# Optimization experiments

Hardware: AMD Instinct MI355X
Metric: run time of the kernel (lower is better)

## Reference

```python
import jax, jax.numpy as jnp
import numpy as np

RANK = 8
ALPHA = 16.0
SCALING = ALPHA / RANK  # LoRA scaling alpha/rank
B, T, P, C = 8, 16, 197, 1024


def setup_inputs() -> dict:
    key = jax.random.key(0)
    k = jax.random.split(key, 8)
    hidden_states = jax.random.normal(k[0], (B, T, P, C), jnp.float32)
    frame_mask = jnp.ones((B, T), jnp.float32)
    # kaiming_uniform_(a=sqrt(5)) on an (out,in) Linear -> U(-1/sqrt(in), 1/sqrt(in))
    s_down = 1.0 / np.sqrt(C).astype(np.float32)
    down_w = jax.random.uniform(k[1], (RANK, C), jnp.float32, -s_down, s_down)
    # PyTorch LSTM default init: U(-1/sqrt(hidden), 1/sqrt(hidden)) for all params
    s_l = 1.0 / np.sqrt(RANK).astype(np.float32)
    w_ih = jax.random.uniform(k[2], (4 * RANK, RANK), jnp.float32, -s_l, s_l)
    w_hh = jax.random.uniform(k[3], (4 * RANK, RANK), jnp.float32, -s_l, s_l)
    b_ih = jax.random.uniform(k[4], (4 * RANK,), jnp.float32, -s_l, s_l)
    b_hh = jax.random.uniform(k[5], (4 * RANK,), jnp.float32, -s_l, s_l)
    # original zero-inits up; use small random so the reference output is non-trivial
    up_w = jax.random.normal(k[6], (C, RANK), jnp.float32) * 0.02
    return {
        "hidden_states": hidden_states,
        "num_frames": T,
        "frame_mask": frame_mask,
        "down_w": down_w,
        "w_ih": w_ih,
        "w_hh": w_hh,
        "b_ih": b_ih,
        "b_hh": b_hh,
        "up_w": up_w,
    }


def _lstm(x, w_ih, w_hh, b_ih, b_hh):
    """Single-layer unidirectional LSTM, PyTorch gate order (i,f,g,o).
    x: (T, N, R) time-major. Returns all hidden states (T, N, R)."""
    n, r = x.shape[1], w_hh.shape[1]
    bias = b_ih + b_hh

    def step(carry, x_t):
        h, c = carry
        gates = x_t @ w_ih.T + h @ w_hh.T + bias  # (N, 4R)
        i, f, g, o = jnp.split(gates, 4, axis=-1)
        c = jax.nn.sigmoid(f) * c + jax.nn.sigmoid(i) * jnp.tanh(g)
        h = jax.nn.sigmoid(o) * jnp.tanh(c)
        return (h, c), h

    init = (jnp.zeros((n, r), x.dtype), jnp.zeros((n, r), x.dtype))
    _, hs = jax.lax.scan(step, init, x)
    return hs


def reference(hidden_states, num_frames, frame_mask, down_w, w_ih, w_hh, b_ih, b_hh, up_w):
    b, t, p, c = hidden_states.shape
    assert t == num_frames
    # LoRA down: (B,T,P,C) x (R,C) -> (B,T,P,R)  (dropout is identity in eval)
    red = jnp.einsum('btpc,rc->btpr', hidden_states, down_w)
    red = red * frame_mask[:, :, None, None]
    # temporal LSTM over T, batch = B*P, in rank space
    seq = red.transpose(1, 0, 2, 3).reshape(t, b * p, -1)  # (T, B*P, R)
    hs = _lstm(seq, w_ih, w_hh, b_ih, b_hh)                # (T, B*P, R)
    out = hs.reshape(t, b, p, -1).transpose(1, 0, 2, 3)    # (B, T, P, R)
    out = out * frame_mask[:, :, None, None]
    # LoRA up + scaling: (B,T,P,R) x (C,R) -> (B,T,P,C)
    delta = jnp.einsum('btpr,or->btpo', out, up_w) * SCALING
    return delta
```

## Files before the change

kernel.cpp:

```cpp
#include <hip/hip_runtime.h>
#include <math.h>

#define BB 8
#define TT 16
#define PP 197
#define CC 1024
#define RR 8
#define NROWS (BB * TT * PP)
#define NSEQ  (BB * PP)
#define LORA_SCALE 2.0f

__device__ __forceinline__ float sigf(float x) {
    x = fminf(fmaxf(x, -30.f), 30.f);
    return 1.0f / (1.0f + __expf(-x));
}
__device__ __forceinline__ float tanh_fast(float x) {
    x = fminf(fmaxf(x, -15.f), 15.f);
    float e = __expf(-2.0f * x);
    return (1.0f - e) / (1.0f + e);
}
__device__ __forceinline__ float dot4(const float4& a, const float4& b) {
    return a.x * b.x + a.y * b.y + a.z * b.z + a.w * b.w;
}

__global__ __launch_bounds__(256) void k_down(const float* __restrict__ hs,
                                              const float* __restrict__ dw,
                                              const float* __restrict__ fm,
                                              float* __restrict__ red) {
    const int lane = threadIdx.x & 63;
    const int wave = (blockIdx.x * blockDim.x + threadIdx.x) >> 6;

    float4 w[RR][4];
#pragma unroll
    for (int r = 0; r < RR; ++r)
#pragma unroll
        for (int k = 0; k < 4; ++k)
            w[r][k] = *(const float4*)(dw + r * CC + k * 256 + lane * 4);

    const int row0 = wave * 2;

    float4 xa[4], xb[4];
    const float* rpa = hs + (size_t)row0 * CC;
    const float* rpb = hs + (size_t)(row0 + 1) * CC;
#pragma unroll
    for (int k = 0; k < 4; ++k) xa[k] = *(const float4*)(rpa + k * 256 + lane * 4);
#pragma unroll
    for (int k = 0; k < 4; ++k) xb[k] = *(const float4*)(rpb + k * 256 + lane * 4);

    float acca[RR], accb[RR];
#pragma unroll
    for (int r = 0; r < RR; ++r) {
        float a = 0.f, b = 0.f;
#pragma unroll
        for (int k = 0; k < 4; ++k) {
            a += dot4(xa[k], w[r][k]);
            b += dot4(xb[k], w[r][k]);
        }
        acca[r] = a; accb[r] = b;
    }
#pragma unroll
    for (int d = 32; d >= 1; d >>= 1) {
#pragma unroll
        for (int r = 0; r < RR; ++r) {
            acca[r] += __shfl_xor(acca[r], d, 64);
            accb[r] += __shfl_xor(accb[r], d, 64);
        }
    }
    if (lane == 0) {
        const float ma = fm[row0 / PP];
        const float mb = fm[(row0 + 1) / PP];
        float4* opa = (float4*)(red + (size_t)row0 * RR);
        float4* opb = (float4*)(red + (size_t)(row0 + 1) * RR);
        opa[0] = make_float4(acca[0] * ma, acca[1] * ma, acca[2] * ma, acca[3] * ma);
        opa[1] = make_float4(acca[4] * ma, acca[5] * ma, acca[6] * ma, acca[7] * ma);
        opb[0] = make_float4(accb[0] * mb, accb[1] * mb, accb[2] * mb, accb[3] * mb);
        opb[1] = make_float4(accb[4] * mb, accb[5] * mb, accb[6] * mb, accb[7] * mb);
    }
}

__global__ __launch_bounds__(256) void k_lstm(const float* __restrict__ red,
                                              const float* __restrict__ fm,
                                              const float* __restrict__ w_ih,
                                              const float* __restrict__ w_hh,
                                              const float* __restrict__ b_ih,
                                              const float* __restrict__ b_hh,
                                              float* __restrict__ hsm) {
    const int tid = blockIdx.x * blockDim.x + threadIdx.x;
    const int n = tid >> 3;
    const int r = tid & 7;
    const int lane = threadIdx.x & 63;
    const int grp = lane & 56;
    const bool valid = (n < NSEQ);

    float wi_i[8], wi_f[8], wi_g[8], wi_o[8];
    float wh_i[8], wh_f[8], wh_g[8], wh_o[8];
#pragma unroll
    for (int j = 0; j < 8; ++j) {
        wi_i[j] = w_ih[(r) * 8 + j];
        wi_f[j] = w_ih[(8 + r) * 8 + j];
        wi_g[j] = w_ih[(16 + r) * 8 + j];
        wi_o[j] = w_ih[(24 + r) * 8 + j];
        wh_i[j] = w_hh[(r) * 8 + j];
        wh_f[j] = w_hh[(8 + r) * 8 + j];
        wh_g[j] = w_hh[(16 + r) * 8 + j];
        wh_o[j] = w_hh[(24 + r) * 8 + j];
    }
    const float bi = b_ih[r] + b_hh[r];
    const float bf = b_ih[8 + r] + b_hh[8 + r];
    const float bg = b_ih[16 + r] + b_hh[16 + r];
    const float bo = b_ih[24 + r] + b_hh[24 + r];

    int b = 0, p = 0;
    if (valid) { b = n / PP; p = n - b * PP; }
    const size_t base = ((size_t)b * TT * PP + p) * RR + r;
    const size_t tstride = (size_t)PP * RR;

    float h = 0.f, c = 0.f;
    for (int t = 0; t < TT; ++t) {
        const float x = valid ? red[base + (size_t)t * tstride] : 0.f;
        float gi = bi, gf = bf, gg = bg, go = bo;
#pragma unroll
        for (int j = 0; j < 8; ++j) {
            const float xv = __shfl(x, grp + j, 64);
            const float hv = __shfl(h, grp + j, 64);
            gi += wi_i[j] * xv + wh_i[j] * hv;
            gf += wi_f[j] * xv + wh_f[j] * hv;
            gg += wi_g[j] * xv + wh_g[j] * hv;
            go += wi_o[j] * xv + wh_o[j] * hv;
        }
        c = sigf(gf) * c + sigf(gi) * tanh_fast(gg);
        h = sigf(go) * tanh_fast(c);
        if (valid) hsm[base + (size_t)t * tstride] = h * fm[b * TT + t];
    }
}

__global__ __launch_bounds__(256) void k_up(const float* __restrict__ hsm,
                                            const float* __restrict__ up,
                                            float* __restrict__ out) {
    const int lane = threadIdx.x & 63;
    const int wave = (blockIdx.x * blockDim.x + threadIdx.x) >> 6;

    float4 u[4][4][2];
#pragma unroll
    for (int k = 0; k < 4; ++k)
#pragma unroll
        for (int j = 0; j < 4; ++j) {
            const float* pp = up + (size_t)(k * 256 + lane * 4 + j) * RR;
            u[k][j][0] = *(const float4*)(pp);
            u[k][j][1] = *(const float4*)(pp + 4);
        }

    const int row0 = wave * 2;
#pragma unroll
    for (int rr = 0; rr < 2; ++rr) {
        const int row = row0 + rr;
        const float* hp = hsm + (size_t)row * RR;
        float4 h0 = *(const float4*)(hp);
        float4 h1 = *(const float4*)(hp + 4);
        h0.x *= LORA_SCALE; h0.y *= LORA_SCALE; h0.z *= LORA_SCALE; h0.w *= LORA_SCALE;
        h1.x *= LORA_SCALE; h1.y *= LORA_SCALE; h1.z *= LORA_SCALE; h1.w *= LORA_SCALE;
        float* op = out + (size_t)row * CC;
#pragma unroll
        for (int k = 0; k < 4; ++k) {
            float4 o;
            o.x = dot4(h0, u[k][0][0]) + dot4(h1, u[k][0][1]);
            o.y = dot4(h0, u[k][1][0]) + dot4(h1, u[k][1][1]);
            o.z = dot4(h0, u[k][2][0]) + dot4(h1, u[k][2][1]);
            o.w = dot4(h0, u[k][3][0]) + dot4(h1, u[k][3][1]);
            *(float4*)(op + k * 256 + lane * 4) = o;
        }
    }
}

extern "C" void kernel_launch(void* const* d_in, const int* in_sizes, int n_in,
                              void* d_out, int out_size, void* d_ws, size_t ws_size,
                              hipStream_t stream) {
    const float* hs  = (const float*)d_in[0];
    const float* fm  = (const float*)d_in[2];
    const float* dw  = (const float*)d_in[3];
    const float* wih = (const float*)d_in[4];
    const float* whh = (const float*)d_in[5];
    const float* bih = (const float*)d_in[6];
    const float* bhh = (const float*)d_in[7];
    const float* up  = (const float*)d_in[8];
    float* out = (float*)d_out;

    float* red = (float*)d_ws;
    float* hsm = red + (size_t)NROWS * RR;

    k_down<<<NROWS / 8, 256, 0, stream>>>(hs, dw, fm, red);
    k_lstm<<<(NSEQ * 8 + 255) / 256, 256, 0, stream>>>(red, fm, wih, whh, bih, bhh, hsm);
    k_up<<<NROWS / 8, 256, 0, stream>>>(hsm, up, out);
}
```

Measured before the change: 257.7 us.

## Use persistent grid-stride loops for down/up kernels and prefetch LSTM inputs

The down and up projection kernels become persistent grid-stride loops over 512 blocks, so weights loaded into registers are reused across many rows instead of reloaded per wave. The up kernel also switches to scalar coalesced stores with a 64-stride column layout. The LSTM kernel uses 64-thread blocks so more CUs run it, and prefetches all 16 timesteps of input and mask into registers before the recurrence. The trade-offs are fewer waves in flight to hide memory latency and narrower stores in the up kernel.

```diff
diff --git a/kernel.cpp b/kernel.cpp
--- a/kernel.cpp
+++ b/kernel.cpp
@@ -7,6 +7,7 @@
 #define CC 1024
 #define RR 8
 #define NROWS (BB * TT * PP)
+#define NPAIRS (NROWS / 2)
 #define NSEQ  (BB * PP)
 #define LORA_SCALE 2.0f
 
@@ -28,7 +29,8 @@
                                               const float* __restrict__ fm,
                                               float* __restrict__ red) {
     const int lane = threadIdx.x & 63;
-    const int wave = (blockIdx.x * blockDim.x + threadIdx.x) >> 6;
+    const int wid  = (blockIdx.x * blockDim.x + threadIdx.x) >> 6;
+    const int nw   = (gridDim.x * blockDim.x) >> 6;
 
     float4 w[RR][4];
 #pragma unroll
@@ -37,60 +39,60 @@
         for (int k = 0; k < 4; ++k)
             w[r][k] = *(const float4*)(dw + r * CC + k * 256 + lane * 4);
 
-    const int row0 = wave * 2;
+    for (int pr = wid; pr < NPAIRS; pr += nw) {
+        const int row0 = pr * 2;
+        float4 xa[4], xb[4];
+        const float* rpa = hs + (size_t)row0 * CC;
+        const float* rpb = rpa + CC;
+#pragma unroll
+        for (int k = 0; k < 4; ++k) xa[k] = *(const float4*)(rpa + k * 256 + lane * 4);
+#pragma unroll
+        for (int k = 0; k < 4; ++k) xb[k] = *(const float4*)(rpb + k * 256 + lane * 4);
 
-    float4 xa[4], xb[4];
-    const float* rpa = hs + (size_t)row0 * CC;
-    const float* rpb = hs + (size_t)(row0 + 1) * CC;
-#pragma unroll
-    for (int k = 0; k < 4; ++k) xa[k] = *(const float4*)(rpa + k * 256 + lane * 4);
-#pragma unroll
-    for (int k = 0; k < 4; ++k) xb[k] = *(const float4*)(rpb + k * 256 + lane * 4);
-
-    float acca[RR], accb[RR];
-#pragma unroll
-    for (int r = 0; r < RR; ++r) {
-        float a = 0.f, b = 0.f;
-#pragma unroll
-        for (int k = 0; k < 4; ++k) {
-            a += dot4(xa[k], w[r][k]);
-            b += dot4(xb[k], w[r][k]);
-        }
-        acca[r] = a; accb[r] = b;
-    }
-#pragma unroll
-    for (int d = 32; d >= 1; d >>= 1) {
+        float acca[RR], accb[RR];
 #pragma unroll
         for (int r = 0; r < RR; ++r) {
-            acca[r] += __shfl_xor(acca[r], d, 64);
-            accb[r] += __shfl_xor(accb[r], d, 64);
+            float a = 0.f, b = 0.f;
+#pragma unroll
+            for (int k = 0; k < 4; ++k) {
+                a += dot4(xa[k], w[r][k]);
+                b += dot4(xb[k], w[r][k]);
+            }
+            acca[r] = a; accb[r] = b;
         }
-    }
-    if (lane == 0) {
-        const float ma = fm[row0 / PP];
-        const float mb = fm[(row0 + 1) / PP];
-        float4* opa = (float4*)(red + (size_t)row0 * RR);
-        float4* opb = (float4*)(red + (size_t)(row0 + 1) * RR);
-        opa[0] = make_float4(acca[0] * ma, acca[1] * ma, acca[2] * ma, acca[3] * ma);
-        opa[1] = make_float4(acca[4] * ma, acca[5] * ma, acca[6] * ma, acca[7] * ma);
-        opb[0] = make_float4(accb[0] * mb, accb[1] * mb, accb[2] * mb, accb[3] * mb);
-        opb[1] = make_float4(accb[4] * mb, accb[5] * mb, accb[6] * mb, accb[7] * mb);
+#pragma unroll
+        for (int d = 32; d >= 1; d >>= 1) {
+#pragma unroll
+            for (int r = 0; r < RR; ++r) {
+                acca[r] += __shfl_xor(acca[r], d, 64);
+                accb[r] += __shfl_xor(accb[r], d, 64);
+            }
+        }
+        if (lane == 0) {
+            const float ma = fm[row0 / PP];
+            const float mb = fm[(row0 + 1) / PP];
+            float4* opa = (float4*)(red + (size_t)row0 * RR);
+            opa[0] = make_float4(acca[0] * ma, acca[1] * ma, acca[2] * ma, acca[3] * ma);
+            opa[1] = make_float4(acca[4] * ma, acca[5] * ma, acca[6] * ma, acca[7] * ma);
+            opa[2] = make_float4(accb[0] * mb, accb[1] * mb, accb[2] * mb, accb[3] * mb);
+            opa[3] = make_float4(accb[4] * mb, accb[5] * mb, accb[6] * mb, accb[7] * mb);
+        }
     }
 }
 
-__global__ __launch_bounds__(256) void k_lstm(const float* __restrict__ red,
-                                              const float* __restrict__ fm,
-                                              const float* __restrict__ w_ih,
-                                              const float* __restrict__ w_hh,
-                                              const float* __restrict__ b_ih,
-                                              const float* __restrict__ b_hh,
-                                              float* __restrict__ hsm) {
+__global__ __launch_bounds__(64) void k_lstm(const float* __restrict__ red,
+                                             const float* __restrict__ fm,
+                                             const float* __restrict__ w_ih,
+                                             const float* __restrict__ w_hh,
+                                             const float* __restrict__ b_ih,
+                                             const float* __restrict__ b_hh,
+                                             float* __restrict__ hsm) {
     const int tid = blockIdx.x * blockDim.x + threadIdx.x;
     const int n = tid >> 3;
     const int r = tid & 7;
     const int lane = threadIdx.x & 63;
     const int grp = lane & 56;
-    const bool valid = (n < NSEQ);
+    if (n >= NSEQ) return;
 
     float wi_i[8], wi_f[8], wi_g[8], wi_o[8];
     float wh_i[8], wh_f[8], wh_g[8], wh_o[8];
@@ -110,18 +112,23 @@
     const float bg = b_ih[16 + r] + b_hh[16 + r];
     const float bo = b_ih[24 + r] + b_hh[24 + r];
 
-    int b = 0, p = 0;
-    if (valid) { b = n / PP; p = n - b * PP; }
+    const int b = n / PP, p = n - (n / PP) * PP;
     const size_t base = ((size_t)b * TT * PP + p) * RR + r;
     const size_t tstride = (size_t)PP * RR;
 
+    float xs[TT], msk[TT];
+#pragma unroll
+    for (int t = 0; t < TT; ++t) xs[t] = red[base + (size_t)t * tstride];
+#pragma unroll
+    for (int t = 0; t < TT; ++t) msk[t] = fm[b * TT + t];
+
     float h = 0.f, c = 0.f;
+#pragma unroll
     for (int t = 0; t < TT; ++t) {
-        const float x = valid ? red[base + (size_t)t * tstride] : 0.f;
         float gi = bi, gf = bf, gg = bg, go = bo;
 #pragma unroll
         for (int j = 0; j < 8; ++j) {
-            const float xv = __shfl(x, grp + j, 64);
+            const float xv = __shfl(xs[t], grp + j, 64);
             const float hv = __shfl(h, grp + j, 64);
             gi += wi_i[j] * xv + wh_i[j] * hv;
             gf += wi_f[j] * xv + wh_f[j] * hv;
@@ -130,7 +137,7 @@
         }
         c = sigf(gf) * c + sigf(gi) * tanh_fast(gg);
         h = sigf(go) * tanh_fast(c);
-        if (valid) hsm[base + (size_t)t * tstride] = h * fm[b * TT + t];
+        hsm[base + (size_t)t * tstride] = h * msk[t];
     }
 }
 
@@ -138,36 +145,27 @@
                                             const float* __restrict__ up,
                                             float* __restrict__ out) {
     const int lane = threadIdx.x & 63;
-    const int wave = (blockIdx.x * blockDim.x + threadIdx.x) >> 6;
+    const int wid  = (blockIdx.x * blockDim.x + threadIdx.x) >> 6;
+    const int nw   = (gridDim.x * blockDim.x) >> 6;
 
-    float4 u[4][4][2];
+    float4 u0[16], u1[16];
 #pragma unroll
-    for (int k = 0; k < 4; ++k)
-#pragma unroll
-        for (int j = 0; j < 4; ++j) {
-            const float* pp = up + (size_t)(k * 256 + lane * 4 + j) * RR;
-            u[k][j][0] = *(const float4*)(pp);
-            u[k][j][1] = *(const float4*)(pp + 4);
-        }
+    for (int g = 0; g < 16; ++g) {
+        const float* pp = up + (size_t)(g * 64 + lane) * RR;
+        u0[g] = *(const float4*)(pp);
+        u1[g] = *(const float4*)(pp + 4);
+    }
 
-    const int row0 = wave * 2;
-#pragma unroll
-    for (int rr = 0; rr < 2; ++rr) {
-        const int row = row0 + rr;
+    for (int row = wid; row < NROWS; row += nw) {
         const float* hp = hsm + (size_t)row * RR;
         float4 h0 = *(const float4*)(hp);
         float4 h1 = *(const float4*)(hp + 4);
         h0.x *= LORA_SCALE; h0.y *= LORA_SCALE; h0.z *= LORA_SCALE; h0.w *= LORA_SCALE;
         h1.x *= LORA_SCALE; h1.y *= LORA_SCALE; h1.z *= LORA_SCALE; h1.w *= LORA_SCALE;
-        float* op = out + (size_t)row * CC;
+        float* op = out + (size_t)row * CC + lane;
 #pragma unroll
-        for (int k = 0; k < 4; ++k) {
-            float4 o;
-            o.x = dot4(h0, u[k][0][0]) + dot4(h1, u[k][0][1]);
-            o.y = dot4(h0, u[k][1][0]) + dot4(h1, u[k][1][1]);
-            o.z = dot4(h0, u[k][2][0]) + dot4(h1, u[k][2][1]);
-            o.w = dot4(h0, u[k][3][0]) + dot4(h1, u[k][3][1]);
-            *(float4*)(op + k * 256 + lane * 4) = o;
+        for (int g = 0; g < 16; ++g) {
+            op[g * 64] = dot4(h0, u0[g]) + dot4(h1, u1[g]);
         }
     }
 }
@@ -188,7 +186,7 @@
     float* red = (float*)d_ws;
     float* hsm = red + (size_t)NROWS * RR;
 
-    k_down<<<NROWS / 8, 256, 0, stream>>>(hs, dw, fm, red);
-    k_lstm<<<(NSEQ * 8 + 255) / 256, 256, 0, stream>>>(red, fm, wih, whh, bih, bhh, hsm);
-    k_up<<<NROWS / 8, 256, 0, stream>>>(hsm, up, out);
+    k_down<<<512, 256, 0, stream>>>(hs, dw, fm, red);
+    k_lstm<<<197, 64, 0, stream>>>(red, fm, wih, whh, bih, bhh, hsm);
+    k_up<<<512, 256, 0, stream>>>(hsm, up, out);
 }
```

Measured after the change: 210.6 us. 1.22x faster.
